# Kernel tuning notes

Hardware: AMD Instinct MI355X
Metric: run time of the kernel (lower is better)

The kernel has to match this reference:

```python
import jax, jax.numpy as jnp
import numpy as np

B, S, D = 2, 192, 256


def _clip_tangent(v, max_norm=4.0):
    n = jnp.linalg.norm(v, axis=-1, keepdims=True) + 1e-8
    return v * jnp.minimum(max_norm / n, 1.0)


def _sq(x):
    return jnp.sum(x * x, axis=-1, keepdims=True)


def _artanh(x):
    return jnp.arctanh(jnp.clip(x, -1.0 + 1e-7, 1.0 - 1e-7))


def _mobius_add(x, y):
    # Poincare ball (c=1) Mobius addition
    x2, y2 = _sq(x), _sq(y)
    xy = jnp.sum(x * y, axis=-1, keepdims=True)
    num = (1.0 + 2.0 * xy + y2) * x + (1.0 - x2) * y
    den = 1.0 + 2.0 * xy + x2 * y2
    return num / jnp.maximum(den, 1e-15)


def _expmap0(v):
    n = jnp.maximum(jnp.linalg.norm(v, axis=-1, keepdims=True), 1e-15)
    return jnp.tanh(n) * v / n


def _logmap0(x):
    n = jnp.maximum(jnp.linalg.norm(x, axis=-1, keepdims=True), 1e-15)
    return _artanh(n) * x / n


def _dist(x, y):
    u = _mobius_add(-x, y)
    return 2.0 * _artanh(jnp.linalg.norm(u, axis=-1))


def _logmap(x, y):
    u = _mobius_add(-x, y)
    un = jnp.maximum(jnp.linalg.norm(u, axis=-1, keepdims=True), 1e-15)
    lam = 2.0 / jnp.maximum(1.0 - _sq(x), 1e-15)
    return (2.0 / lam) * _artanh(un) * u / un


def _expmap(x, v):
    n = jnp.maximum(jnp.linalg.norm(v, axis=-1, keepdims=True), 1e-15)
    lam = 2.0 / jnp.maximum(1.0 - _sq(x), 1e-15)
    return _mobius_add(x, jnp.tanh(lam * n / 2.0) * v / n)


def _projx(x):
    n = jnp.linalg.norm(x, axis=-1, keepdims=True)
    maxn = 1.0 - 1e-5
    return jnp.where(n > maxn, x * maxn / jnp.maximum(n, 1e-15), x)


def _normalize(v, axis, eps=1e-8):
    return v / jnp.maximum(jnp.linalg.norm(v, axis=axis, keepdims=True), eps)


def setup_inputs() -> dict:
    key = jax.random.key(0)
    ks = jax.random.split(key, 8)

    def lin_w(k):
        return 0.02 * jax.random.normal(k, (D, D), jnp.float32)

    return {
        'q_in': 0.1 * jax.random.normal(ks[0], (B, S, D), jnp.float32),
        'k_in': 0.1 * jax.random.normal(ks[1], (B, S, D), jnp.float32),
        'v_in': 0.1 * jax.random.normal(ks[2], (B, S, D), jnp.float32),
        'Wq': lin_w(ks[3]), 'bq': jnp.zeros((D,), jnp.float32),
        'Wk': lin_w(ks[4]), 'bk': jnp.zeros((D,), jnp.float32),
        'Wv': lin_w(ks[5]), 'bv': jnp.zeros((D,), jnp.float32),
        'Wo': lin_w(ks[6]), 'bo': jnp.zeros((D,), jnp.float32),
        'tau': jnp.asarray(0.02, jnp.float32),
        'tangent_scale': jnp.asarray(1.0, jnp.float32),
    }


def _forward(q_in, k_in, v_in, Wq, bq, Wk, bk, Wv, bv, Wo, bo, tau, tangent_scale):
    nk = jax.random.split(jax.random.key(42), 3)  # deterministic stand-in for randn_like noise
    q = q_in @ Wq.T + bq
    k = k_in @ Wk.T + bk
    v = v_in @ Wv.T + bv

    q_hyp = _expmap0(_clip_tangent(q))
    k_hyp = _expmap0(_clip_tangent(k))

    # pairwise hyperbolic distance attention: [B,S,S]
    dist_matrix = _dist(q_hyp[:, :, None, :], k_hyp[:, None, :, :])
    min_dist = jnp.min(dist_matrix, axis=-1, keepdims=True)
    w_unnorm = jnp.exp(-(dist_matrix - min_dist))
    w_probs = w_unnorm / (jnp.sum(w_unnorm, axis=-1, keepdims=True) + 1e-8)
    h = jnp.einsum('bqs,bsd->bqd', w_probs, v)

    # differentiable Karcher flow (3-step Riemannian SGD for Frechet mean)
    wn = w_unnorm / (jnp.sum(w_unnorm, axis=-1, keepdims=True) + 1e-8)
    mu_hyp = _expmap0(_clip_tangent(jnp.einsum('bqs,bsd->bqd', wn, k)))
    k_hyp2 = _expmap0(_clip_tangent(k))
    for _ in range(3):
        log_k = _logmap(mu_hyp[:, :, None, :], k_hyp2[:, None, :, :])  # [B,S,S,D]
        v_grad = jnp.sum(wn[..., None] * log_k, axis=2)
        mu_hyp = _expmap(mu_hyp, _clip_tangent(0.1 * v_grad))

    noise = 1e-5 * jax.random.normal(nk[0], mu_hyp.shape, mu_hyp.dtype)
    k_centroid = _projx(mu_hyp + noise)

    c2k = _dist(k_centroid[:, :, None, :], k_hyp[:, None, :, :])  # [B,S,S]
    wv = w_unnorm / (jnp.sum(w_unnorm, axis=-1, keepdims=True) + 1e-8)
    entropy = -jnp.sum(wv * jnp.log(wv + 1e-8), axis=-1, keepdims=True)
    effective_mass = jnp.exp(entropy)
    variance = jnp.sum(wv * c2k ** 2, axis=-1, keepdims=True)
    tension = variance - tau * effective_mass  # [B,S,1]

    # local tangent frame + power iteration for principal direction
    k_local = _logmap(k_centroid[:, :, None, :], k_hyp[:, None, :, :])  # [B,S,S,D]
    weighted_k = k_local * jnp.sqrt(w_unnorm[..., None] + 1e-8)
    v_rand = jax.random.normal(nk[1], (B, S, D, 1), weighted_k.dtype)
    v_rand = _normalize(v_rand, axis=2)
    for _ in range(3):
        proj = jnp.einsum('bqsd,bqdo->bqso', weighted_k, v_rand)
        v_rand = _normalize(jnp.einsum('bqsd,bqso->bqdo', weighted_k, proj), axis=2)
    w_local = v_rand[..., 0]
    # transp0back(x, v) = v * lambda_x / 2 = v / (1 - ||x||^2)
    w_global = w_local / jnp.maximum(1.0 - _sq(k_centroid), 1e-15)
    fallback = _normalize(_logmap0(q_hyp) - _logmap0(k_centroid), axis=-1)
    w_proj = jnp.where(variance > 1e-5, w_global, fallback)

    h_norm = jnp.linalg.norm(h, axis=-1, keepdims=True)
    h_comp = jnp.arcsinh(h_norm) * h / (h_norm + 1e-8)

    # Pitchfork bifurcation ODE, RK4: dx/dt = tension*x - x^3
    x = jnp.sum(h_comp * w_proj, axis=-1, keepdims=True)
    ode_noise = 1e-4 * jax.random.normal(nk[2], x.shape, x.dtype)
    xi = jnp.where(x == 0, ode_noise, x)
    dt = 0.5
    f = lambda z: tension * z - z ** 3
    for _ in range(4):
        k1 = dt * f(xi)
        k2 = dt * f(xi + k1 / 2)
        k3 = dt * f(xi + k2 / 2)
        k4 = dt * f(xi + k3)
        xi = xi + (k1 + 2 * k2 + 2 * k3 + k4) / 6.0
    h_prime = h_comp + (xi - x) * w_proj
    h_prime_hyp = _expmap0(_clip_tangent(h_prime * tangent_scale))
    h_out_bif = _logmap0(h_prime_hyp)

    tau_safe = jnp.maximum(tau, 1e-3)
    gate = jnp.maximum(jnp.tanh(tension / tau_safe), 0.0)
    h_fused = (1.0 - gate) * h + gate * h_out_bif
    return h_fused @ Wo.T + bo


def reference(q_in, k_in, v_in, Wq, bq, Wk, bk, Wv, bv, Wo, bo, tau, tangent_scale):
    return _forward(q_in, k_in, v_in, Wq, bq, Wk, bk, Wv, bv, Wo, bo, tau, tangent_scale)
```

## Files before the change

kernel.cpp:

```cpp
#include <hip/hip_runtime.h>
#include <hip/hip_bf16.h>
#include <stdint.h>

#define BB 2
#define SS 192
#define DD 256
#define NROW (BB * SS)
#define NE (NROW * DD)

__device__ __forceinline__ uint32_t rotl32(uint32_t v, int d) {
  return (v << d) | (v >> (32 - d));
}

__device__ inline void threefry2x32(uint32_t k0, uint32_t k1, uint32_t x0, uint32_t x1,
                                    uint32_t* o0, uint32_t* o1) {
  uint32_t ks2 = k0 ^ k1 ^ 0x1BD11BDAu;
  x0 += k0; x1 += k1;
  const int ra[4] = {13, 15, 26, 6};
  const int rb[4] = {17, 29, 16, 24};
#pragma unroll
  for (int i = 0; i < 4; i++) { x0 += x1; x1 = rotl32(x1, ra[i]); x1 ^= x0; }
  x0 += k1; x1 += ks2 + 1u;
#pragma unroll
  for (int i = 0; i < 4; i++) { x0 += x1; x1 = rotl32(x1, rb[i]); x1 ^= x0; }
// ... 41 lines not shown

__device__ inline float jax_normal_from_bits(uint32_t bits) {
  float f = __uint_as_float((bits >> 9) | 0x3f800000u) - 1.0f;
  const float lo = -0.99999994f;
  float u = f * (1.0f - lo) + lo;
  u = fmaxf(lo, u);
  return 1.4142135623730951f * erfinv_xla_f32(u);
}

__device__ inline float jax_normal_at(uint32_t ka, uint32_t kb, uint32_t i) {
  uint32_t o0, o1;
  threefry2x32(ka, kb, 0u, i, &o0, &o1);
  return jax_normal_from_bits(o0 ^ o1);
}

__device__ inline double blockSum(double v, double* red, int tid) {
#pragma unroll
  for (int o = 32; o > 0; o >>= 1) v += __shfl_down(v, o, 64);
  __syncthreads();
  if ((tid & 63) == 0) red[tid >> 6] = v;
  __syncthreads();
  return (red[0] + red[1]) + (red[2] + red[3]);
}

__device__ inline double reduceS_sum(const double* arr, double* red, int tid) {
  __syncthreads();
  if (tid < 64) {
    double v = arr[tid] + arr[tid + 64] + arr[tid + 128];
#pragma unroll
    for (int o = 32; o > 0; o >>= 1) v += __shfl_down(v, o, 64);
    if (tid == 0) red[4] = v;
  }
  __syncthreads();
  return red[4];
}

__device__ inline double reduceS_min(const double* arr, double* red, int tid) {
  __syncthreads();
  if (tid < 64) {
    double v = fmin(arr[tid], fmin(arr[tid + 64], arr[tid + 128]));
#pragma unroll
    for (int o = 32; o > 0; o >>= 1) v = fmin(v, __shfl_down(v, o, 64));
    if (tid == 0) red[5] = v;
  }
  __syncthreads();
  return red[5];
}

#define SDOT(vecLds, khTp, outv) do {                                        \
    const float* cb_ = (khTp) + tid;                                         \
    double s0_=0.0,s1_=0.0,s2_=0.0,s3_=0.0,s4_=0.0,s5_=0.0,s6_=0.0,s7_=0.0;  \
    for (int d0_ = 0; d0_ < DD; d0_ += 8) {                                  \
      float f0_ = cb_[(size_t)(d0_ + 0) * SS];                               \
      float f1_ = cb_[(size_t)(d0_ + 1) * SS];                               \
      float f2_ = cb_[(size_t)(d0_ + 2) * SS];                               \
      float f3_ = cb_[(size_t)(d0_ + 3) * SS];                               \
      float f4_ = cb_[(size_t)(d0_ + 4) * SS];                               \
      float f5_ = cb_[(size_t)(d0_ + 5) * SS];                               \
      float f6_ = cb_[(size_t)(d0_ + 6) * SS];                               \
      float f7_ = cb_[(size_t)(d0_ + 7) * SS];                               \
      s0_ += (vecLds)[d0_ + 0] * (double)f0_;                                \
      s1_ += (vecLds)[d0_ + 1] * (double)f1_;                                \
      s2_ += (vecLds)[d0_ + 2] * (double)f2_;                                \
      s3_ += (vecLds)[d0_ + 3] * (double)f3_;                                \
      s4_ += (vecLds)[d0_ + 4] * (double)f4_;                                \
      s5_ += (vecLds)[d0_ + 5] * (double)f5_;                                \
      s6_ += (vecLds)[d0_ + 6] * (double)f6_;                                \
      s7_ += (vecLds)[d0_ + 7] * (double)f7_;                                \
    }                                                                        \
    (outv) = ((s0_ + s1_) + (s2_ + s3_)) + ((s4_ + s5_) + (s6_ + s7_));      \
  } while (0)

#define DSUM(wArr, mat, outv) do {                                           \
    const float* mb_ = (mat) + tid;                                          \
    double s0_=0.0,s1_=0.0,s2_=0.0,s3_=0.0,s4_=0.0,s5_=0.0,s6_=0.0,s7_=0.0;  \
    for (int t0_ = 0; t0_ < SS; t0_ += 8) {                                  \
      float f0_ = mb_[(size_t)(t0_ + 0) * DD];                               \
      float f1_ = mb_[(size_t)(t0_ + 1) * DD];                               \
      float f2_ = mb_[(size_t)(t0_ + 2) * DD];                               \
      float f3_ = mb_[(size_t)(t0_ + 3) * DD];                               \
      float f4_ = mb_[(size_t)(t0_ + 4) * DD];                               \
      float f5_ = mb_[(size_t)(t0_ + 5) * DD];                               \
      float f6_ = mb_[(size_t)(t0_ + 6) * DD];                               \
      float f7_ = mb_[(size_t)(t0_ + 7) * DD];                               \
      s0_ += (wArr)[t0_ + 0] * (double)f0_;                                  \
      s1_ += (wArr)[t0_ + 1] * (double)f1_;                                  \
      s2_ += (wArr)[t0_ + 2] * (double)f2_;                                  \
      s3_ += (wArr)[t0_ + 3] * (double)f3_;                                  \
      s4_ += (wArr)[t0_ + 4] * (double)f4_;                                  \
      s5_ += (wArr)[t0_ + 5] * (double)f5_;                                  \
      s6_ += (wArr)[t0_ + 6] * (double)f6_;                                  \
      s7_ += (wArr)[t0_ + 7] * (double)f7_;                                  \
    }                                                                        \
    (outv) = ((s0_ + s1_) + (s2_ + s3_)) + ((s4_ + s5_) + (s6_ + s7_));      \
  } while (0)

__global__ void transpose4(const float* __restrict__ Wq, const float* __restrict__ Wk,
                           const float* __restrict__ Wv, const float* __restrict__ Wo,
                           float* __restrict__ WqT, float* __restrict__ WkT,
                           float* __restrict__ WvT, float* __restrict__ WoT) {
  int m = blockIdx.x >> 8;
  int i = blockIdx.x & 255;
  int j = threadIdx.x;
  const float* S_; float* D_;
  if (m == 0) { S_ = Wq; D_ = WqT; }
  else if (m == 1) { S_ = Wk; D_ = WkT; }
  else if (m == 2) { S_ = Wv; D_ = WvT; }
  else { S_ = Wo; D_ = WoT; }
  D_[i * DD + j] = S_[j * DD + i];
}

__device__ inline double colDot(const float* __restrict__ xs,
                                const float* __restrict__ WT, int j) {
  const float* cb = WT + j;
  double s0=0.0,s1=0.0,s2=0.0,s3=0.0,s4=0.0,s5=0.0,s6=0.0,s7=0.0;
  for (int i0 = 0; i0 < DD; i0 += 8) {
    float f0 = cb[(size_t)(i0 + 0) * DD];
    float f1 = cb[(size_t)(i0 + 1) * DD];
    float f2 = cb[(size_t)(i0 + 2) * DD];
    float f3 = cb[(size_t)(i0 + 3) * DD];
    float f4 = cb[(size_t)(i0 + 4) * DD];
    float f5 = cb[(size_t)(i0 + 5) * DD];
    float f6 = cb[(size_t)(i0 + 6) * DD];
    float f7 = cb[(size_t)(i0 + 7) * DD];
    s0 += (double)xs[i0 + 0] * (double)f0;
    s1 += (double)xs[i0 + 1] * (double)f1;
    s2 += (double)xs[i0 + 2] * (double)f2;
    s3 += (double)xs[i0 + 3] * (double)f3;
    s4 += (double)xs[i0 + 4] * (double)f4;
    s5 += (double)xs[i0 + 5] * (double)f5;
    s6 += (double)xs[i0 + 6] * (double)f6;
    s7 += (double)xs[i0 + 7] * (double)f7;
  }
  return ((s0 + s1) + (s2 + s3)) + ((s4 + s5) + (s6 + s7));
}

__global__ __launch_bounds__(256) void proj_kernel(
    const float* __restrict__ q_in, const float* __restrict__ k_in, const float* __restrict__ v_in,
    const float* __restrict__ WqT, const float* __restrict__ WkT, const float* __restrict__ WvT,
    const float* __restrict__ bq, const float* __restrict__ bk, const float* __restrict__ bv,
    float* __restrict__ qh, float* __restrict__ kb, float* __restrict__ vb,
    float* __restrict__ kh, float* __restrict__ khT, double* __restrict__ y2g) {
  const int row = blockIdx.x, m = blockIdx.y, j = threadIdx.x;
  __shared__ float xs[DD];
  __shared__ double red[8];
  const float* x; const float* WT; const float* bias;
  if (m == 0) { x = q_in; WT = WqT; bias = bq; }
  else if (m == 1) { x = k_in; WT = WkT; bias = bk; }
  else { x = v_in; WT = WvT; bias = bv; }
  xs[j] = x[(size_t)row * DD + j];
  __syncthreads();
// ... 14 lines not shown
    kh[(size_t)row * DD + j] = khf;
    int bb = row / SS, s = row % SS;
    khT[((size_t)bb * DD + j) * SS + s] = khf;
    double y2 = blockSum((double)khf * (double)khf, red, j);
    if (j == 0) y2g[row] = y2;
  }
}

__global__ __launch_bounds__(256) void resonance_main(
    const float* __restrict__ q_hyp, const float* __restrict__ k_hyp,
    const float* __restrict__ k_hypT, const float* __restrict__ kmat,
    const float* __restrict__ vmat, const double* __restrict__ y2g,
    const float* __restrict__ WoT, const float* __restrict__ bo,
    const float* __restrict__ tau_p, const float* __restrict__ ts_p,
    float* __restrict__ out) {
  __shared__ double xq[DD], xc[DD], vr[DD];
  __shared__ double y2s[SS], wun[SS], wns[SS], alf[SS], bet[SS], sA[SS], sB[SS];
  __shared__ float hfl[DD];
  __shared__ double red[8];
  const int tid = threadIdx.x;
  const int blk = blockIdx.x;
  const int b = blk / SS;
  const size_t rowOff = (size_t)blk * DD;
  const float* khB = k_hyp + (size_t)b * SS * DD;
  const float* khT = k_hypT + (size_t)b * DD * SS;
  const float* kB = kmat + (size_t)b * SS * DD;
  const float* vB = vmat + (size_t)b * SS * DD;

  uint32_t nk0a, nk0b, nk1a, nk1b, nk2a, nk2b;
  threefry2x32(0u, 42u, 0u, 0u, &nk0a, &nk0b);
  threefry2x32(0u, 42u, 0u, 1u, &nk1a, &nk1b);
  threefry2x32(0u, 42u, 0u, 2u, &nk2a, &nk2b);
  const uint32_t ei = (uint32_t)(rowOff + tid);
  const double noiseval = 1e-5 * (double)jax_normal_at(nk0a, nk0b, ei);
  const double vrndval = (double)jax_normal_at(nk1a, nk1b, ei);
  const double odeval = 1e-4 * (double)jax_normal_at(nk2a, nk2b, (uint32_t)blk);

  double xqv = (double)q_hyp[rowOff + tid];
  xq[tid] = xqv;
  if (tid < SS) y2s[tid] = y2g[b * SS + tid];
  double x2q = blockSum(xqv * xqv, red, tid);

  if (tid < SS) {
    double dot;
    SDOT(xq, khT, dot);
    double y2 = y2s[tid];
    double A = 1.0 - 2.0 * dot + y2;
    double Dn = fmax(1.0 - 2.0 * dot + x2q * y2, 1e-15);
    double Bc = 1.0 - x2q;
    double u2 = (A * A * x2q - 2.0 * A * Bc * dot + Bc * Bc * y2) / (Dn * Dn);
    double unr = sqrt(fmax(u2, 0.0));
    sA[tid] = 2.0 * atanh(fmin(unr, 1.0 - 1e-7));
  }
  double mind = reduceS_min(sA, red, tid);
  if (tid < SS) wun[tid] = exp(-(sA[tid] - mind));
  double wsum = reduceS_sum(wun, red, tid);
  if (tid < SS) wns[tid] = wun[tid] * (1.0 / (wsum + 1e-8));
  __syncthreads();

  double hreg, mu;
  {
    const float* vb_ = vB + tid;
    const float* kb_ = kB + tid;
    double h0=0.0,h1=0.0,h2=0.0,h3=0.0, m0=0.0,m1=0.0,m2=0.0,m3=0.0;
    for (int s0 = 0; s0 < SS; s0 += 4) {
      float v0 = vb_[(size_t)(s0 + 0) * DD];
      float v1 = vb_[(size_t)(s0 + 1) * DD];
      float v2 = vb_[(size_t)(s0 + 2) * DD];
      float v3 = vb_[(size_t)(s0 + 3) * DD];
      float k0 = kb_[(size_t)(s0 + 0) * DD];
      float k1 = kb_[(size_t)(s0 + 1) * DD];
      float k2 = kb_[(size_t)(s0 + 2) * DD];
      float k3 = kb_[(size_t)(s0 + 3) * DD];
      double w0 = wns[s0 + 0], w1 = wns[s0 + 1], w2 = wns[s0 + 2], w3 = wns[s0 + 3];
      h0 += w0 * (double)v0; h1 += w1 * (double)v1;
      h2 += w2 * (double)v2; h3 += w3 * (double)v3;
      m0 += w0 * (double)k0; m1 += w1 * (double)k1;
      m2 += w2 * (double)k2; m3 += w3 * (double)k3;
    }
    hreg = (h0 + h1) + (h2 + h3);
    mu = (m0 + m1) + (m2 + m3);
  }

  double x2c;
  {
    double n2 = blockSum(mu * mu, red, tid);
    double n = sqrt(n2);
    double cf = fmin(4.0 / (n + 1e-8), 1.0);
    double ncl = fmax(n * cf, 1e-15);
    double th = tanh(ncl);
    xc[tid] = mu * (th * cf / ncl);
    x2c = th * th;
  }
  __syncthreads();

  for (int it = 0; it < 3; ++it) {
    if (tid < SS) {
      double dot;
      SDOT(xc, khT, dot);
      double y2 = y2s[tid];
      double A = 1.0 - 2.0 * dot + y2;
      double Dn = fmax(1.0 - 2.0 * dot + x2c * y2, 1e-15);
      double Bc = 1.0 - x2c;
      double u2 = (A * A * x2c - 2.0 * A * Bc * dot + Bc * Bc * y2) / (Dn * Dn);
      double unr = sqrt(fmax(u2, 0.0));
      double un = fmax(unr, 1e-15);
      double coef = fmax(Bc, 1e-15) * atanh(fmin(un, 1.0 - 1e-7)) / un;
      double cs = wns[tid] * coef / Dn;
      sA[tid] = cs;
      sB[tid] = cs * A;
    }
    double S1 = reduceS_sum(sB, red, tid);
    double g;
    DSUM(sA, khB, g);
    double xold = xc[tid];
    double Bc = 1.0 - x2c;
    double vg = Bc * g - S1 * xold;
    double nv2 = blockSum(vg * vg, red, tid);
    double nv = 0.1 * sqrt(nv2);
    double cf = fmin(4.0 / (nv + 1e-8), 1.0);
    double nw = fmax(nv * cf, 1e-15);
    double tsc = tanh(nw / fmax(Bc, 1e-15));
    double zco = tsc * 0.1 * cf / nw;
    double z = zco * vg;
    double xz = blockSum(xold * z, red, tid);
    double z2 = tsc * tsc;
    double den = fmax(1.0 + 2.0 * xz + x2c * z2, 1e-15);
    double xnew = ((1.0 + 2.0 * xz + z2) * xold + (1.0 - x2c) * z) / den;
    xc[tid] = xnew;
    x2c = blockSum(xnew * xnew, red, tid);
  }

  {
    double cn = xc[tid] + noiseval;
    double n2 = blockSum(cn * cn, red, tid);
    double nn = sqrt(n2);
    if (nn > 1.0 - 1e-5) cn *= (1.0 - 1e-5) / fmax(nn, 1e-15);
    xc[tid] = cn;
    x2c = blockSum(cn * cn, red, tid);
  }

  if (tid < SS) {
    double dot;
    SDOT(xc, khT, dot);
    double y2 = y2s[tid];
    double A = 1.0 - 2.0 * dot + y2;
    double Dn = fmax(1.0 - 2.0 * dot + x2c * y2, 1e-15);
    double Bc = 1.0 - x2c;
    double u2 = (A * A * x2c - 2.0 * A * Bc * dot + Bc * Bc * y2) / (Dn * Dn);
    double unr = sqrt(fmax(u2, 0.0));
    double c2k = 2.0 * atanh(fmin(unr, 1.0 - 1e-7));
    sA[tid] = wns[tid] * c2k * c2k;
    sB[tid] = -wns[tid] * log(wns[tid] + 1e-8);
    double un = fmax(unr, 1e-15);
    double gl = fmax(Bc, 1e-15) * atanh(fmin(un, 1.0 - 1e-7)) / (un * Dn);
    double sq = sqrt(wun[tid] + 1e-8);
    alf[tid] = -sq * gl * A;
    bet[tid] = sq * gl * Bc;
  }
  double variance = reduceS_sum(sA, red, tid);
  double entropy = reduceS_sum(sB, red, tid);
  double tau = (double)tau_p[0];
  double tension = variance - tau * exp(entropy);

  {
    double n2 = blockSum(vrndval * vrndval, red, tid);
    vr[tid] = vrndval / fmax(sqrt(n2), 1e-8);
  }
  for (int it = 0; it < 3; ++it) {
    double dxv = blockSum(xc[tid] * vr[tid], red, tid);
    if (tid < SS) {
      double dot;
      SDOT(vr, khT, dot);
      double pj = alf[tid] * dxv + bet[tid] * dot;
      sA[tid] = alf[tid] * pj;
      sB[tid] = bet[tid] * pj;
    }
    double T1 = reduceS_sum(sA, red, tid);
    double g;
    DSUM(sB, khB, g);
    double vnew = T1 * xc[tid] + g;
    double n2 = blockSum(vnew * vnew, red, tid);
    vr[tid] = vnew / fmax(sqrt(n2), 1e-8);
  }

  double wproj;
  {
    double wg = vr[tid] / fmax(1.0 - x2c, 1e-15);
    double nq = fmax(sqrt(x2q), 1e-15);
    double aq = atanh(fmin(nq, 1.0 - 1e-7)) / nq;
    double nc = fmax(sqrt(x2c), 1e-15);
    double ac = atanh(fmin(nc, 1.0 - 1e-7)) / nc;
    double f = aq * xq[tid] - ac * xc[tid];
    double n2 = blockSum(f * f, red, tid);
    double fb = f / fmax(sqrt(n2), 1e-8);
    wproj = (variance > 1e-5) ? wg : fb;
  }

  double hn2 = blockSum(hreg * hreg, red, tid);
  double hn = sqrt(hn2);
  double hsc = asinh(hn) / (hn + 1e-8);
  double hc = hsc * hreg;
  double x = blockSum(hc * wproj, red, tid);
  double xi = (x == 0.0) ? odeval : x;
  const double dt = 0.5;
#pragma unroll
  for (int r = 0; r < 4; ++r) {
    double k1 = dt * (tension * xi - xi * xi * xi);
    double a2 = xi + 0.5 * k1;
    double k2 = dt * (tension * a2 - a2 * a2 * a2);
    double a3 = xi + 0.5 * k2;
    double k3 = dt * (tension * a3 - a3 * a3 * a3);
    double a4 = xi + k3;
    double k4 = dt * (tension * a4 - a4 * a4 * a4);
    xi += (k1 + 2.0 * k2 + 2.0 * k3 + k4) / 6.0;
  }
  double ts = (double)ts_p[0];
  double hp = (hc + (xi - x) * wproj) * ts;
  double hp2 = blockSum(hp * hp, red, tid);
  double nhp = sqrt(hp2);
  double cf = fmin(4.0 / (nhp + 1e-8), 1.0);
  double ncl = fmax(nhp * cf, 1e-15);
  double th = tanh(ncl);
  double nb = fmax(th, 1e-15);
  double ab = atanh(fmin(nb, 1.0 - 1e-7)) / nb;
  double hob = ab * th * cf / ncl * hp;
  double gate = fmax(tanh(tension / fmax(tau, 1e-3)), 0.0);

  hfl[tid] = (float)((1.0 - gate) * hreg + gate * hob);
  __syncthreads();
  double o = colDot(hfl, WoT, tid) + (double)bo[tid];
  out[rowOff + tid] = (float)o;
}

extern "C" void kernel_launch(void* const* d_in, const int* in_sizes, int n_in,
                              void* d_out, int out_size, void* d_ws, size_t ws_size,
                              hipStream_t stream) {
  const float* q_in = (const float*)d_in[0];
  const float* k_in = (const float*)d_in[1];
  const float* v_in = (const float*)d_in[2];
  const float* Wq = (const float*)d_in[3];
  const float* bq = (const float*)d_in[4];
  const float* Wk = (const float*)d_in[5];
  const float* bk = (const float*)d_in[6];
  const float* Wv = (const float*)d_in[7];
  const float* bv = (const float*)d_in[8];
  const float* Wo = (const float*)d_in[9];
// ... 14 lines not shown
  float* WkT = (float*)alloc((size_t)DD * DD * 4);
  float* WvT = (float*)alloc((size_t)DD * DD * 4);
  float* WoT = (float*)alloc((size_t)DD * DD * 4);
  float* kb = (float*)alloc((size_t)NE * 4);
  float* vb = (float*)alloc((size_t)NE * 4);
  float* qh = (float*)alloc((size_t)NE * 4);
  float* kh = (float*)alloc((size_t)NE * 4);
  float* khT = (float*)alloc((size_t)NE * 4);
  double* y2g = (double*)alloc((size_t)NROW * 8);

  hipLaunchKernelGGL(transpose4, dim3(4 * DD), dim3(DD), 0, stream,
                     Wq, Wk, Wv, Wo, WqT, WkT, WvT, WoT);
  hipLaunchKernelGGL(proj_kernel, dim3(NROW, 3), dim3(DD), 0, stream,
                     q_in, k_in, v_in, WqT, WkT, WvT, bq, bk, bv,
                     qh, kb, vb, kh, khT, y2g);
  hipLaunchKernelGGL(resonance_main, dim3(NROW), dim3(DD), 0, stream,
                     qh, kh, khT, kb, vb, y2g, WoT, bo, tau, ts, out);
}
```

Before: 144.3 us.

## Process two query rows per block in resonance kernel to share key loads

The main kernel now handles two adjacent query rows per block, so every load of the key, value and weight matrices feeds two sets of accumulators. Reductions are paired, which halves the number of barriers per row. The aim is to cut global/L2 traffic on the memory-bound dot products and amortise synchronisation. The cost is half as many blocks (192 instead of 384), higher register and LDS pressure, and lower occupancy on a GPU with many CUs.

```diff
diff --git a/kernel.cpp b/kernel.cpp
--- a/kernel.cpp
+++ b/kernel.cpp
@@ -79,42 +79,58 @@
   return jax_normal_from_bits(o0 ^ o1);
 }
 
-__device__ inline double blockSum(double v, double* red, int tid) {
-#pragma unroll
-  for (int o = 32; o > 0; o >>= 1) v += __shfl_down(v, o, 64);
-  __syncthreads();
-  if ((tid & 63) == 0) red[tid >> 6] = v;
-  __syncthreads();
-  return (red[0] + red[1]) + (red[2] + red[3]);
-}
-
-__device__ inline double reduceS_sum(const double* arr, double* red, int tid) {
+__device__ inline void blockSum2(double vA, double vB, double* red, int tid,
+                                 double& oA, double& oB) {
+#pragma unroll
+  for (int o = 32; o > 0; o >>= 1) {
+    vA += __shfl_down(vA, o, 64);
+    vB += __shfl_down(vB, o, 64);
+  }
+  __syncthreads();
+  if ((tid & 63) == 0) { red[tid >> 6] = vA; red[4 + (tid >> 6)] = vB; }
+  __syncthreads();
+  oA = (red[0] + red[1]) + (red[2] + red[3]);
+  oB = (red[4] + red[5]) + (red[6] + red[7]);
+}
+
+__device__ inline void reduceS_sum2(const double* aA, const double* aB, double* red,
+                                    int tid, double& oA, double& oB) {
   __syncthreads();
   if (tid < 64) {
-    double v = arr[tid] + arr[tid + 64] + arr[tid + 128];
-#pragma unroll
-    for (int o = 32; o > 0; o >>= 1) v += __shfl_down(v, o, 64);
-    if (tid == 0) red[4] = v;
-  }
-  __syncthreads();
-  return red[4];
-}
-
-__device__ inline double reduceS_min(const double* arr, double* red, int tid) {
+    double vA = aA[tid] + aA[tid + 64] + aA[tid + 128];
+    double vB = aB[tid] + aB[tid + 64] + aB[tid + 128];
+#pragma unroll
+    for (int o = 32; o > 0; o >>= 1) {
+      vA += __shfl_down(vA, o, 64);
+      vB += __shfl_down(vB, o, 64);
+    }
+    if (tid == 0) { red[8] = vA; red[9] = vB; }
+  }
+  __syncthreads();
+  oA = red[8]; oB = red[9];
+}
+
+__device__ inline void reduceS_min2(const double* aA, const double* aB, double* red,
+                                    int tid, double& oA, double& oB) {
   __syncthreads();
   if (tid < 64) {
-    double v = fmin(arr[tid], fmin(arr[tid + 64], arr[tid + 128]));
-#pragma unroll
-    for (int o = 32; o > 0; o >>= 1) v = fmin(v, __shfl_down(v, o, 64));
-    if (tid == 0) red[5] = v;
-  }
-  __syncthreads();
-  return red[5];
-}
-
-#define SDOT(vecLds, khTp, outv) do {                                        \
+    double vA = fmin(aA[tid], fmin(aA[tid + 64], aA[tid + 128]));
+    double vB = fmin(aB[tid], fmin(aB[tid + 64], aB[tid + 128]));
+#pragma unroll
+    for (int o = 32; o > 0; o >>= 1) {
+      vA = fmin(vA, __shfl_down(vA, o, 64));
+      vB = fmin(vB, __shfl_down(vB, o, 64));
+    }
+    if (tid == 0) { red[10] = vA; red[11] = vB; }
+  }
+  __syncthreads();
+  oA = red[10]; oB = red[11];
+}
+
+#define SDOT2(vLA, vLB, khTp, outA, outB) do {                               \
     const float* cb_ = (khTp) + tid;                                         \
-    double s0_=0.0,s1_=0.0,s2_=0.0,s3_=0.0,s4_=0.0,s5_=0.0,s6_=0.0,s7_=0.0;  \
+    double a0_=0,a1_=0,a2_=0,a3_=0,a4_=0,a5_=0,a6_=0,a7_=0;                  \
+    double b0_=0,b1_=0,b2_=0,b3_=0,b4_=0,b5_=0,b6_=0,b7_=0;                  \
     for (int d0_ = 0; d0_ < DD; d0_ += 8) {                                  \
       float f0_ = cb_[(size_t)(d0_ + 0) * SS];                               \
       float f1_ = cb_[(size_t)(d0_ + 1) * SS];                               \
@@ -124,21 +140,23 @@
       float f5_ = cb_[(size_t)(d0_ + 5) * SS];                               \
       float f6_ = cb_[(size_t)(d0_ + 6) * SS];                               \
       float f7_ = cb_[(size_t)(d0_ + 7) * SS];                               \
-      s0_ += (vecLds)[d0_ + 0] * (double)f0_;                                \
-      s1_ += (vecLds)[d0_ + 1] * (double)f1_;                                \
-      s2_ += (vecLds)[d0_ + 2] * (double)f2_;                                \
-      s3_ += (vecLds)[d0_ + 3] * (double)f3_;                                \
-      s4_ += (vecLds)[d0_ + 4] * (double)f4_;                                \
-      s5_ += (vecLds)[d0_ + 5] * (double)f5_;                                \
-      s6_ += (vecLds)[d0_ + 6] * (double)f6_;                                \
-      s7_ += (vecLds)[d0_ + 7] * (double)f7_;                                \
+      a0_ += (vLA)[d0_ + 0] * (double)f0_;  b0_ += (vLB)[d0_ + 0] * (double)f0_; \
+      a1_ += (vLA)[d0_ + 1] * (double)f1_;  b1_ += (vLB)[d0_ + 1] * (double)f1_; \
+      a2_ += (vLA)[d0_ + 2] * (double)f2_;  b2_ += (vLB)[d0_ + 2] * (double)f2_; \
+      a3_ += (vLA)[d0_ + 3] * (double)f3_;  b3_ += (vLB)[d0_ + 3] * (double)f3_; \
+      a4_ += (vLA)[d0_ + 4] * (double)f4_;  b4_ += (vLB)[d0_ + 4] * (double)f4_; \
+      a5_ += (vLA)[d0_ + 5] * (double)f5_;  b5_ += (vLB)[d0_ + 5] * (double)f5_; \
+      a6_ += (vLA)[d0_ + 6] * (double)f6_;  b6_ += (vLB)[d0_ + 6] * (double)f6_; \
+      a7_ += (vLA)[d0_ + 7] * (double)f7_;  b7_ += (vLB)[d0_ + 7] * (double)f7_; \
     }                                                                        \
-    (outv) = ((s0_ + s1_) + (s2_ + s3_)) + ((s4_ + s5_) + (s6_ + s7_));      \
+    (outA) = ((a0_ + a1_) + (a2_ + a3_)) + ((a4_ + a5_) + (a6_ + a7_));      \
+    (outB) = ((b0_ + b1_) + (b2_ + b3_)) + ((b4_ + b5_) + (b6_ + b7_));      \
   } while (0)
 
-#define DSUM(wArr, mat, outv) do {                                           \
-    const float* mb_ = (mat) + tid;                                          \
-    double s0_=0.0,s1_=0.0,s2_=0.0,s3_=0.0,s4_=0.0,s5_=0.0,s6_=0.0,s7_=0.0;  \
+#define DSUM2(wA, wB, mat, outA, outB) do {                                  \
+    const float* mb_ = (mat);                                                \
+    double a0_=0,a1_=0,a2_=0,a3_=0,a4_=0,a5_=0,a6_=0,a7_=0;                  \
+    double b0_=0,b1_=0,b2_=0,b3_=0,b4_=0,b5_=0,b6_=0,b7_=0;                  \
     for (int t0_ = 0; t0_ < SS; t0_ += 8) {                                  \
       float f0_ = mb_[(size_t)(t0_ + 0) * DD];                               \
       float f1_ = mb_[(size_t)(t0_ + 1) * DD];                               \
@@ -148,16 +166,17 @@
       float f5_ = mb_[(size_t)(t0_ + 5) * DD];                               \
       float f6_ = mb_[(size_t)(t0_ + 6) * DD];                               \
       float f7_ = mb_[(size_t)(t0_ + 7) * DD];                               \
-      s0_ += (wArr)[t0_ + 0] * (double)f0_;                                  \
-      s1_ += (wArr)[t0_ + 1] * (double)f1_;                                  \
-      s2_ += (wArr)[t0_ + 2] * (double)f2_;                                  \
-      s3_ += (wArr)[t0_ + 3] * (double)f3_;                                  \
-      s4_ += (wArr)[t0_ + 4] * (double)f4_;                                  \
-      s5_ += (wArr)[t0_ + 5] * (double)f5_;                                  \
-      s6_ += (wArr)[t0_ + 6] * (double)f6_;                                  \
-      s7_ += (wArr)[t0_ + 7] * (double)f7_;                                  \
+      a0_ += (wA)[t0_ + 0] * (double)f0_;  b0_ += (wB)[t0_ + 0] * (double)f0_; \
+      a1_ += (wA)[t0_ + 1] * (double)f1_;  b1_ += (wB)[t0_ + 1] * (double)f1_; \
+      a2_ += (wA)[t0_ + 2] * (double)f2_;  b2_ += (wB)[t0_ + 2] * (double)f2_; \
+      a3_ += (wA)[t0_ + 3] * (double)f3_;  b3_ += (wB)[t0_ + 3] * (double)f3_; \
+      a4_ += (wA)[t0_ + 4] * (double)f4_;  b4_ += (wB)[t0_ + 4] * (double)f4_; \
+      a5_ += (wA)[t0_ + 5] * (double)f5_;  b5_ += (wB)[t0_ + 5] * (double)f5_; \
+      a6_ += (wA)[t0_ + 6] * (double)f6_;  b6_ += (wB)[t0_ + 6] * (double)f6_; \
+      a7_ += (wA)[t0_ + 7] * (double)f7_;  b7_ += (wB)[t0_ + 7] * (double)f7_; \
     }                                                                        \
-    (outv) = ((s0_ + s1_) + (s2_ + s3_)) + ((s4_ + s5_) + (s6_ + s7_));      \
+    (outA) = ((a0_ + a1_) + (a2_ + a3_)) + ((a4_ + a5_) + (a6_ + a7_));      \
+    (outB) = ((b0_ + b1_) + (b2_ + b3_)) + ((b4_ + b5_) + (b6_ + b7_));      \
   } while (0)
 
 __global__ void transpose4(const float* __restrict__ Wq, const float* __restrict__ Wk,
@@ -173,6 +192,15 @@
   else if (m == 2) { S_ = Wv; D_ = WvT; }
   else { S_ = Wo; D_ = WoT; }
   D_[i * DD + j] = S_[j * DD + i];
+}
+
+__device__ inline double blockSum(double v, double* red, int tid) {
+#pragma unroll
+  for (int o = 32; o > 0; o >>= 1) v += __shfl_down(v, o, 64);
+  __syncthreads();
+  if ((tid & 63) == 0) red[tid >> 6] = v;
+  __syncthreads();
+  return (red[0] + red[1]) + (red[2] + red[3]);
 }
 
 __device__ inline double colDot(const float* __restrict__ xs,
@@ -200,6 +228,25 @@
   return ((s0 + s1) + (s2 + s3)) + ((s4 + s5) + (s6 + s7));
 }
 
+__device__ inline void colDot2(const float* __restrict__ xsA, const float* __restrict__ xsB,
+                               const float* __restrict__ WT, int j,
+                               double& oA, double& oB) {
+  const float* cb = WT + j;
+  double a0=0,a1=0,a2=0,a3=0, b0=0,b1=0,b2=0,b3=0;
+  for (int i0 = 0; i0 < DD; i0 += 4) {
+    float f0 = cb[(size_t)(i0 + 0) * DD];
+    float f1 = cb[(size_t)(i0 + 1) * DD];
+    float f2 = cb[(size_t)(i0 + 2) * DD];
+    float f3 = cb[(size_t)(i0 + 3) * DD];
+    a0 += (double)xsA[i0 + 0] * (double)f0;  b0 += (double)xsB[i0 + 0] * (double)f0;
+    a1 += (double)xsA[i0 + 1] * (double)f1;  b1 += (double)xsB[i0 + 1] * (double)f1;
+    a2 += (double)xsA[i0 + 2] * (double)f2;  b2 += (double)xsB[i0 + 2] * (double)f2;
+    a3 += (double)xsA[i0 + 3] * (double)f3;  b3 += (double)xsB[i0 + 3] * (double)f3;
+  }
+  oA = (a0 + a1) + (a2 + a3);
+  oB = (b0 + b1) + (b2 + b3);
+}
+
 __global__ __launch_bounds__(256) void proj_kernel(
     const float* __restrict__ q_in, const float* __restrict__ k_in, const float* __restrict__ v_in,
     const float* __restrict__ WqT, const float* __restrict__ WkT, const float* __restrict__ WvT,
@@ -244,14 +291,19 @@
     const float* __restrict__ WoT, const float* __restrict__ bo,
     const float* __restrict__ tau_p, const float* __restrict__ ts_p,
     float* __restrict__ out) {
-  __shared__ double xq[DD], xc[DD], vr[DD];
-  __shared__ double y2s[SS], wun[SS], wns[SS], alf[SS], bet[SS], sA[SS], sB[SS];
-  __shared__ float hfl[DD];
-  __shared__ double red[8];
+  __shared__ double xqA[DD], xqB[DD], xcA[DD], xcB[DD], vrA[DD], vrB[DD];
+  __shared__ double y2s[SS];
+  __shared__ double wunA[SS], wunB[SS], wnsA[SS], wnsB[SS];
+  __shared__ double alfA[SS], alfB[SS], betA[SS], betB[SS];
+  __shared__ double sAA[SS], sAB[SS], sBA[SS], sBB[SS];
+  __shared__ float hflA[DD], hflB[DD];
+  __shared__ double red[16];
   const int tid = threadIdx.x;
-  const int blk = blockIdx.x;
-  const int b = blk / SS;
-  const size_t rowOff = (size_t)blk * DD;
+  const int pblk = blockIdx.x;
+  const int b = pblk / (SS / 2);
+  const int qp = pblk % (SS / 2);
+  const int rowA = b * SS + 2 * qp, rowB = rowA + 1;
+  const size_t offA = (size_t)rowA * DD, offB = (size_t)rowB * DD;
   const float* khB = k_hyp + (size_t)b * SS * DD;
   const float* khT = k_hypT + (size_t)b * DD * SS;
   const float* kB = kmat + (size_t)b * SS * DD;
@@ -261,38 +313,61 @@
   threefry2x32(0u, 42u, 0u, 0u, &nk0a, &nk0b);
   threefry2x32(0u, 42u, 0u, 1u, &nk1a, &nk1b);
   threefry2x32(0u, 42u, 0u, 2u, &nk2a, &nk2b);
-  const uint32_t ei = (uint32_t)(rowOff + tid);
-  const double noiseval = 1e-5 * (double)jax_normal_at(nk0a, nk0b, ei);
-  const double vrndval = (double)jax_normal_at(nk1a, nk1b, ei);
-  const double odeval = 1e-4 * (double)jax_normal_at(nk2a, nk2b, (uint32_t)blk);
-
-  double xqv = (double)q_hyp[rowOff + tid];
-  xq[tid] = xqv;
+  const double noiseA = 1e-5 * (double)jax_normal_at(nk0a, nk0b, (uint32_t)(offA + tid));
+  const double noiseB = 1e-5 * (double)jax_normal_at(nk0a, nk0b, (uint32_t)(offB + tid));
+  const double vrndA = (double)jax_normal_at(nk1a, nk1b, (uint32_t)(offA + tid));
+  const double vrndB = (double)jax_normal_at(nk1a, nk1b, (uint32_t)(offB + tid));
+  const double odeA = 1e-4 * (double)jax_normal_at(nk2a, nk2b, (uint32_t)rowA);
+  const double odeB = 1e-4 * (double)jax_normal_at(nk2a, nk2b, (uint32_t)rowB);
+
+  double xqvA = (double)q_hyp[offA + tid];
+  double xqvB = (double)q_hyp[offB + tid];
+  xqA[tid] = xqvA;
+  xqB[tid] = xqvB;
   if (tid < SS) y2s[tid] = y2g[b * SS + tid];
-  double x2q = blockSum(xqv * xqv, red, tid);
+  double x2qA, x2qB;
+  blockSum2(xqvA * xqvA, xqvB * xqvB, red, tid, x2qA, x2qB);
 
   if (tid < SS) {
-    double dot;
-    SDOT(xq, khT, dot);
+    double dA, dB;
+    SDOT2(xqA, xqB, khT, dA, dB);
     double y2 = y2s[tid];
-    double A = 1.0 - 2.0 * dot + y2;
-    double Dn = fmax(1.0 - 2.0 * dot + x2q * y2, 1e-15);
-    double Bc = 1.0 - x2q;
-    double u2 = (A * A * x2q - 2.0 * A * Bc * dot + Bc * Bc * y2) / (Dn * Dn);
-    double unr = sqrt(fmax(u2, 0.0));
-    sA[tid] = 2.0 * atanh(fmin(unr, 1.0 - 1e-7));
-  }
-  double mind = reduceS_min(sA, red, tid);
-  if (tid < SS) wun[tid] = exp(-(sA[tid] - mind));
-  double wsum = reduceS_sum(wun, red, tid);
-  if (tid < SS) wns[tid] = wun[tid] * (1.0 / (wsum + 1e-8));
-  __syncthreads();
-
-  double hreg, mu;
+    {
+      double A = 1.0 - 2.0 * dA + y2;
+      double Dn = fmax(1.0 - 2.0 * dA + x2qA * y2, 1e-15);
+      double Bc = 1.0 - x2qA;
+      double u2 = (A * A * x2qA - 2.0 * A * Bc * dA + Bc * Bc * y2) / (Dn * Dn);
+      double unr = sqrt(fmax(u2, 0.0));
+      sAA[tid] = 2.0 * atanh(fmin(unr, 1.0 - 1e-7));
+    }
+    {
+      double A = 1.0 - 2.0 * dB + y2;
+      double Dn = fmax(1.0 - 2.0 * dB + x2qB * y2, 1e-15);
+      double Bc = 1.0 - x2qB;
+      double u2 = (A * A * x2qB - 2.0 * A * Bc * dB + Bc * Bc * y2) / (Dn * Dn);
+      double unr = sqrt(fmax(u2, 0.0));
+      sAB[tid] = 2.0 * atanh(fmin(unr, 1.0 - 1e-7));
+    }
+  }
+  double mindA, mindB;
+  reduceS_min2(sAA, sAB, red, tid, mindA, mindB);
+  if (tid < SS) {
+    wunA[tid] = exp(-(sAA[tid] - mindA));
+    wunB[tid] = exp(-(sAB[tid] - mindB));
+  }
+  double wsA, wsB;
+  reduceS_sum2(wunA, wunB, red, tid, wsA, wsB);
+  if (tid < SS) {
+    wnsA[tid] = wunA[tid] * (1.0 / (wsA + 1e-8));
+    wnsB[tid] = wunB[tid] * (1.0 / (wsB + 1e-8));
+  }
+  __syncthreads();
+
+  double hregA, hregB, muA, muB;
   {
     const float* vb_ = vB + tid;
     const float* kb_ = kB + tid;
-    double h0=0.0,h1=0.0,h2=0.0,h3=0.0, m0=0.0,m1=0.0,m2=0.0,m3=0.0;
+    double hA0=0,hA1=0,hB0=0,hB1=0, mA0=0,mA1=0,mB0=0,mB1=0;
     for (int s0 = 0; s0 < SS; s0 += 4) {
       float v0 = vb_[(size_t)(s0 + 0) * DD];
       float v1 = vb_[(size_t)(s0 + 1) * DD];
@@ -302,165 +377,291 @@
       float k1 = kb_[(size_t)(s0 + 1) * DD];
       float k2 = kb_[(size_t)(s0 + 2) * DD];
       float k3 = kb_[(size_t)(s0 + 3) * DD];
-      double w0 = wns[s0 + 0], w1 = wns[s0 + 1], w2 = wns[s0 + 2], w3 = wns[s0 + 3];
-      h0 += w0 * (double)v0; h1 += w1 * (double)v1;
-      h2 += w2 * (double)v2; h3 += w3 * (double)v3;
-      m0 += w0 * (double)k0; m1 += w1 * (double)k1;
-      m2 += w2 * (double)k2; m3 += w3 * (double)k3;
-    }
-    hreg = (h0 + h1) + (h2 + h3);
-    mu = (m0 + m1) + (m2 + m3);
-  }
-
-  double x2c;
+      double wA0 = wnsA[s0 + 0], wA1 = wnsA[s0 + 1], wA2 = wnsA[s0 + 2], wA3 = wnsA[s0 + 3];
+      double wB0 = wnsB[s0 + 0], wB1 = wnsB[s0 + 1], wB2 = wnsB[s0 + 2], wB3 = wnsB[s0 + 3];
+      hA0 += wA0 * (double)v0; hB0 += wB0 * (double)v0;
+      mA0 += wA0 * (double)k0; mB0 += wB0 * (double)k0;
+      hA1 += wA1 * (double)v1; hB1 += wB1 * (double)v1;
+      mA1 += wA1 * (double)k1; mB1 += wB1 * (double)k1;
+      hA0 += wA2 * (double)v2; hB0 += wB2 * (double)v2;
+      mA0 += wA2 * (double)k2; mB0 += wB2 * (double)k2;
+      hA1 += wA3 * (double)v3; hB1 += wB3 * (double)v3;
+      mA1 += wA3 * (double)k3; mB1 += wB3 * (double)k3;
+    }
+    hregA = hA0 + hA1; hregB = hB0 + hB1;
+    muA = mA0 + mA1;   muB = mB0 + mB1;
+  }
+
+  double x2cA, x2cB;
   {
-    double n2 = blockSum(mu * mu, red, tid);
-    double n = sqrt(n2);
-    double cf = fmin(4.0 / (n + 1e-8), 1.0);
-    double ncl = fmax(n * cf, 1e-15);
-    double th = tanh(ncl);
-    xc[tid] = mu * (th * cf / ncl);
-    x2c = th * th;
+    double n2A, n2B;
+    blockSum2(muA * muA, muB * muB, red, tid, n2A, n2B);
+    {
+      double n = sqrt(n2A);
+      double cf = fmin(4.0 / (n + 1e-8), 1.0);
+      double ncl = fmax(n * cf, 1e-15);
+      double th = tanh(ncl);
+      xcA[tid] = muA * (th * cf / ncl);
+      x2cA = th * th;
+    }
+    {
+      double n = sqrt(n2B);
+      double cf = fmin(4.0 / (n + 1e-8), 1.0);
+      double ncl = fmax(n * cf, 1e-15);
+      double th = tanh(ncl);
+      xcB[tid] = muB * (th * cf / ncl);
+      x2cB = th * th;
+    }
   }
   __syncthreads();
 
   for (int it = 0; it < 3; ++it) {
     if (tid < SS) {
-      double dot;
-      SDOT(xc, khT, dot);
+      double dA, dB;
+      SDOT2(xcA, xcB, khT, dA, dB);
       double y2 = y2s[tid];
-      double A = 1.0 - 2.0 * dot + y2;
-      double Dn = fmax(1.0 - 2.0 * dot + x2c * y2, 1e-15);
-      double Bc = 1.0 - x2c;
-      double u2 = (A * A * x2c - 2.0 * A * Bc * dot + Bc * Bc * y2) / (Dn * Dn);
+      {
+        double A = 1.0 - 2.0 * dA + y2;
+        double Dn = fmax(1.0 - 2.0 * dA + x2cA * y2, 1e-15);
+        double Bc = 1.0 - x2cA;
+        double u2 = (A * A * x2cA - 2.0 * A * Bc * dA + Bc * Bc * y2) / (Dn * Dn);
+        double unr = sqrt(fmax(u2, 0.0));
+        double un = fmax(unr, 1e-15);
+        double coef = fmax(Bc, 1e-15) * atanh(fmin(un, 1.0 - 1e-7)) / un;
+        double cs = wnsA[tid] * coef / Dn;
+        sAA[tid] = cs;
+        sBA[tid] = cs * A;
+      }
+      {
+        double A = 1.0 - 2.0 * dB + y2;
+        double Dn = fmax(1.0 - 2.0 * dB + x2cB * y2, 1e-15);
+        double Bc = 1.0 - x2cB;
+        double u2 = (A * A * x2cB - 2.0 * A * Bc * dB + Bc * Bc * y2) / (Dn * Dn);
+        double unr = sqrt(fmax(u2, 0.0));
+        double un = fmax(unr, 1e-15);
+        double coef = fmax(Bc, 1e-15) * atanh(fmin(un, 1.0 - 1e-7)) / un;
+        double cs = wnsB[tid] * coef / Dn;
+        sAB[tid] = cs;
+        sBB[tid] = cs * A;
+      }
+    }
+    double S1A, S1B;
+    reduceS_sum2(sBA, sBB, red, tid, S1A, S1B);
+    double gA, gB;
+    DSUM2(sAA, sAB, khB + tid, gA, gB);
+    double xoldA = xcA[tid], xoldB = xcB[tid];
+    double BcA = 1.0 - x2cA, BcB = 1.0 - x2cB;
+    double vgA = BcA * gA - S1A * xoldA;
+    double vgB = BcB * gB - S1B * xoldB;
+    double nv2A, nv2B;
+    blockSum2(vgA * vgA, vgB * vgB, red, tid, nv2A, nv2B);
+    double zA, z2A, zB, z2B;
+    {
+      double nv = 0.1 * sqrt(nv2A);
+      double cf = fmin(4.0 / (nv + 1e-8), 1.0);
+      double nw = fmax(nv * cf, 1e-15);
+      double tsc = tanh(nw / fmax(BcA, 1e-15));
+      zA = tsc * 0.1 * cf / nw * vgA;
+      z2A = tsc * tsc;
+    }
+    {
+      double nv = 0.1 * sqrt(nv2B);
+      double cf = fmin(4.0 / (nv + 1e-8), 1.0);
+      double nw = fmax(nv * cf, 1e-15);
+      double tsc = tanh(nw / fmax(BcB, 1e-15));
+      zB = tsc * 0.1 * cf / nw * vgB;
+      z2B = tsc * tsc;
+    }
+    double xzA, xzB;
+    blockSum2(xoldA * zA, xoldB * zB, red, tid, xzA, xzB);
+    double xnewA = ((1.0 + 2.0 * xzA + z2A) * xoldA + (1.0 - x2cA) * zA) /
+                   fmax(1.0 + 2.0 * xzA + x2cA * z2A, 1e-15);
+    double xnewB = ((1.0 + 2.0 * xzB + z2B) * xoldB + (1.0 - x2cB) * zB) /
+                   fmax(1.0 + 2.0 * xzB + x2cB * z2B, 1e-15);
+    xcA[tid] = xnewA;
+    xcB[tid] = xnewB;
+    blockSum2(xnewA * xnewA, xnewB * xnewB, red, tid, x2cA, x2cB);
+  }
+
+  {
+    double cnA = xcA[tid] + noiseA;
+    double cnB = xcB[tid] + noiseB;
+    double n2A, n2B;
+    blockSum2(cnA * cnA, cnB * cnB, red, tid, n2A, n2B);
+    double nnA = sqrt(n2A), nnB = sqrt(n2B);
+    if (nnA > 1.0 - 1e-5) cnA *= (1.0 - 1e-5) / fmax(nnA, 1e-15);
+    if (nnB > 1.0 - 1e-5) cnB *= (1.0 - 1e-5) / fmax(nnB, 1e-15);
+    xcA[tid] = cnA;
+    xcB[tid] = cnB;
+    blockSum2(cnA * cnA, cnB * cnB, red, tid, x2cA, x2cB);
+  }
+
+  if (tid < SS) {
+    double dA, dB;
+    SDOT2(xcA, xcB, khT, dA, dB);
+    double y2 = y2s[tid];
+    {
+      double A = 1.0 - 2.0 * dA + y2;
+      double Dn = fmax(1.0 - 2.0 * dA + x2cA * y2, 1e-15);
+      double Bc = 1.0 - x2cA;
+      double u2 = (A * A * x2cA - 2.0 * A * Bc * dA + Bc * Bc * y2) / (Dn * Dn);
       double unr = sqrt(fmax(u2, 0.0));
+      double c2k = 2.0 * atanh(fmin(unr, 1.0 - 1e-7));
+      sAA[tid] = wnsA[tid] * c2k * c2k;
+      sBA[tid] = -wnsA[tid] * log(wnsA[tid] + 1e-8);
       double un = fmax(unr, 1e-15);
-      double coef = fmax(Bc, 1e-15) * atanh(fmin(un, 1.0 - 1e-7)) / un;
-      double cs = wns[tid] * coef / Dn;
-      sA[tid] = cs;
-      sB[tid] = cs * A;
-    }
-    double S1 = reduceS_sum(sB, red, tid);
-    double g;
-    DSUM(sA, khB, g);
-    double xold = xc[tid];
-    double Bc = 1.0 - x2c;
-    double vg = Bc * g - S1 * xold;
-    double nv2 = blockSum(vg * vg, red, tid);
-    double nv = 0.1 * sqrt(nv2);
-    double cf = fmin(4.0 / (nv + 1e-8), 1.0);
-    double nw = fmax(nv * cf, 1e-15);
-    double tsc = tanh(nw / fmax(Bc, 1e-15));
-    double zco = tsc * 0.1 * cf / nw;
-    double z = zco * vg;
-    double xz = blockSum(xold * z, red, tid);
-    double z2 = tsc * tsc;
-    double den = fmax(1.0 + 2.0 * xz + x2c * z2, 1e-15);
-    double xnew = ((1.0 + 2.0 * xz + z2) * xold + (1.0 - x2c) * z) / den;
-    xc[tid] = xnew;
-    x2c = blockSum(xnew * xnew, red, tid);
-  }
+      double gl = fmax(Bc, 1e-15) * atanh(fmin(un, 1.0 - 1e-7)) / (un * Dn);
+      double sq = sqrt(wunA[tid] + 1e-8);
+      alfA[tid] = -sq * gl * A;
+      betA[tid] = sq * gl * Bc;
+    }
+    {
+      double A = 1.0 - 2.0 * dB + y2;
+      double Dn = fmax(1.0 - 2.0 * dB + x2cB * y2, 1e-15);
+      double Bc = 1.0 - x2cB;
+      double u2 = (A * A * x2cB - 2.0 * A * Bc * dB + Bc * Bc * y2) / (Dn * Dn);
+      double unr = sqrt(fmax(u2, 0.0));
+      double c2k = 2.0 * atanh(fmin(unr, 1.0 - 1e-7));
+      sAB[tid] = wnsB[tid] * c2k * c2k;
+      sBB[tid] = -wnsB[tid] * log(wnsB[tid] + 1e-8);
+      double un = fmax(unr, 1e-15);
+      double gl = fmax(Bc, 1e-15) * atanh(fmin(un, 1.0 - 1e-7)) / (un * Dn);
+      double sq = sqrt(wunB[tid] + 1e-8);
+      alfB[tid] = -sq * gl * A;
+      betB[tid] = sq * gl * Bc;
+    }
+  }
+  double varA, varB, entA, entB;
+  reduceS_sum2(sAA, sAB, red, tid, varA, varB);
+  reduceS_sum2(sBA, sBB, red, tid, entA, entB);
+  double tau = (double)tau_p[0];
+  double tensionA = varA - tau * exp(entA);
+  double tensionB = varB - tau * exp(entB);
 
   {
-    double cn = xc[tid] + noiseval;
-    double n2 = blockSum(cn * cn, red, tid);
-    double nn = sqrt(n2);
-    if (nn > 1.0 - 1e-5) cn *= (1.0 - 1e-5) / fmax(nn, 1e-15);
-    xc[tid] = cn;
-    x2c = blockSum(cn * cn, red, tid);
-  }
-
-  if (tid < SS) {
-    double dot;
-    SDOT(xc, khT, dot);
-    double y2 = y2s[tid];
-    double A = 1.0 - 2.0 * dot + y2;
-    double Dn = fmax(1.0 - 2.0 * dot + x2c * y2, 1e-15);
-    double Bc = 1.0 - x2c;
-    double u2 = (A * A * x2c - 2.0 * A * Bc * dot + Bc * Bc * y2) / (Dn * Dn);
-    double unr = sqrt(fmax(u2, 0.0));
-    double c2k = 2.0 * atanh(fmin(unr, 1.0 - 1e-7));
-    sA[tid] = wns[tid] * c2k * c2k;
-    sB[tid] = -wns[tid] * log(wns[tid] + 1e-8);
-    double un = fmax(unr, 1e-15);
-    double gl = fmax(Bc, 1e-15) * atanh(fmin(un, 1.0 - 1e-7)) / (un * Dn);
-    double sq = sqrt(wun[tid] + 1e-8);
-    alf[tid] = -sq * gl * A;
-    bet[tid] = sq * gl * Bc;
-  }
-  double variance = reduceS_sum(sA, red, tid);
-  double entropy = reduceS_sum(sB, red, tid);
-  double tau = (double)tau_p[0];
-  double tension = variance - tau * exp(entropy);
-
+    double n2A, n2B;
+    blockSum2(vrndA * vrndA, vrndB * vrndB, red, tid, n2A, n2B);
+    vrA[tid] = vrndA / fmax(sqrt(n2A), 1e-8);
+    vrB[tid] = vrndB / fmax(sqrt(n2B), 1e-8);
+  }
+  for (int it = 0; it < 3; ++it) {
+    double dxvA, dxvB;
+    blockSum2(xcA[tid] * vrA[tid], xcB[tid] * vrB[tid], red, tid, dxvA, dxvB);
+    if (tid < SS) {
+      double dA, dB;
+      SDOT2(vrA, vrB, khT, dA, dB);
+      double pjA = alfA[tid] * dxvA + betA[tid] * dA;
+      double pjB = alfB[tid] * dxvB + betB[tid] * dB;
+      sAA[tid] = alfA[tid] * pjA;
+      sBA[tid] = betA[tid] * pjA;
+      sAB[tid] = alfB[tid] * pjB;
+      sBB[tid] = betB[tid] * pjB;
+    }
+    double T1A, T1B;
+    reduceS_sum2(sAA, sAB, red, tid, T1A, T1B);
+    double gA, gB;
+    DSUM2(sBA, sBB, khB + tid, gA, gB);
+    double vnewA = T1A * xcA[tid] + gA;
+    double vnewB = T1B * xcB[tid] + gB;
+    double n2A, n2B;
+    blockSum2(vnewA * vnewA, vnewB * vnewB, red, tid, n2A, n2B);
+    vrA[tid] = vnewA / fmax(sqrt(n2A), 1e-8);
+    vrB[tid] = vnewB / fmax(sqrt(n2B), 1e-8);
+  }
+
+  double wprojA, wprojB;
   {
-    double n2 = blockSum(vrndval * vrndval, red, tid);
-    vr[tid] = vrndval / fmax(sqrt(n2), 1e-8);
-  }
-  for (int it = 0; it < 3; ++it) {
-    double dxv = blockSum(xc[tid] * vr[tid], red, tid);
-    if (tid < SS) {
-      double dot;
-      SDOT(vr, khT, dot);
-      double pj = alf[tid] * dxv + bet[tid] * dot;
-      sA[tid] = alf[tid] * pj;
-      sB[tid] = bet[tid] * pj;
-    }
-    double T1 = reduceS_sum(sA, red, tid);
-    double g;
-    DSUM(sB, khB, g);
-    double vnew = T1 * xc[tid] + g;
-    double n2 = blockSum(vnew * vnew, red, tid);
-    vr[tid] = vnew / fmax(sqrt(n2), 1e-8);
-  }
-
-  double wproj;
+    double fA, fB;
+    {
+      double nq = fmax(sqrt(x2qA), 1e-15);
+      double aq = atanh(fmin(nq, 1.0 - 1e-7)) / nq;
+      double nc = fmax(sqrt(x2cA), 1e-15);
+      double ac = atanh(fmin(nc, 1.0 - 1e-7)) / nc;
+      fA = aq * xqA[tid] - ac * xcA[tid];
+    }
+    {
+      double nq = fmax(sqrt(x2qB), 1e-15);
+      double aq = atanh(fmin(nq, 1.0 - 1e-7)) / nq;
+      double nc = fmax(sqrt(x2cB), 1e-15);
+      double ac = atanh(fmin(nc, 1.0 - 1e-7)) / nc;
+      fB = aq * xqB[tid] - ac * xcB[tid];
+    }
+    double n2A, n2B;
+    blockSum2(fA * fA, fB * fB, red, tid, n2A, n2B);
+    double wgA = vrA[tid] / fmax(1.0 - x2cA, 1e-15);
+    double wgB = vrB[tid] / fmax(1.0 - x2cB, 1e-15);
+    wprojA = (varA > 1e-5) ? wgA : (fA / fmax(sqrt(n2A), 1e-8));
+    wprojB = (varB > 1e-5) ? wgB : (fB / fmax(sqrt(n2B), 1e-8));
+  }
+
+  double hn2A, hn2B;
+  blockSum2(hregA * hregA, hregB * hregB, red, tid, hn2A, hn2B);
+  double hnA = sqrt(hn2A), hnB = sqrt(hn2B);
+  double hcA = asinh(hnA) / (hnA + 1e-8) * hregA;
+  double hcB = asinh(hnB) / (hnB + 1e-8) * hregB;
+  double xA, xB;
+  blockSum2(hcA * wprojA, hcB * wprojB, red, tid, xA, xB);
+  double xiA = (xA == 0.0) ? odeA : xA;
+  double xiB = (xB == 0.0) ? odeB : xB;
+  const double dt = 0.5;
+#pragma unroll
+  for (int r = 0; r < 4; ++r) {
+    {
+      double k1 = dt * (tensionA * xiA - xiA * xiA * xiA);
+      double a2 = xiA + 0.5 * k1;
+      double k2 = dt * (tensionA * a2 - a2 * a2 * a2);
+      double a3 = xiA + 0.5 * k2;
+      double k3 = dt * (tensionA * a3 - a3 * a3 * a3);
+      double a4 = xiA + k3;
+      double k4 = dt * (tensionA * a4 - a4 * a4 * a4);
+      xiA += (k1 + 2.0 * k2 + 2.0 * k3 + k4) / 6.0;
+    }
+    {
+      double k1 = dt * (tensionB * xiB - xiB * xiB * xiB);
+      double a2 = xiB + 0.5 * k1;
+      double k2 = dt * (tensionB * a2 - a2 * a2 * a2);
+      double a3 = xiB + 0.5 * k2;
+      double k3 = dt * (tensionB * a3 - a3 * a3 * a3);
+      double a4 = xiB + k3;
+      double k4 = dt * (tensionB * a4 - a4 * a4 * a4);
+      xiB += (k1 + 2.0 * k2 + 2.0 * k3 + k4) / 6.0;
+    }
+  }
+  double ts = (double)ts_p[0];
+  double hpA = (hcA + (xiA - xA) * wprojA) * ts;
+  double hpB = (hcB + (xiB - xB) * wprojB) * ts;
+  double hp2A, hp2B;
+  blockSum2(hpA * hpA, hpB * hpB, red, tid, hp2A, hp2B);
+  double hobA, hobB;
   {
-    double wg = vr[tid] / fmax(1.0 - x2c, 1e-15);
-    double nq = fmax(sqrt(x2q), 1e-15);
-    double aq = atanh(fmin(nq, 1.0 - 1e-7)) / nq;
-    double nc = fmax(sqrt(x2c), 1e-15);
-    double ac = atanh(fmin(nc, 1.0 - 1e-7)) / nc;
-    double f = aq * xq[tid] - ac * xc[tid];
-    double n2 = blockSum(f * f, red, tid);
-    double fb = f / fmax(sqrt(n2), 1e-8);
-    wproj = (variance > 1e-5) ? wg : fb;
-  }
-
-  double hn2 = blockSum(hreg * hreg, red, tid);
-  double hn = sqrt(hn2);
-  double hsc = asinh(hn) / (hn + 1e-8);
-  double hc = hsc * hreg;
-  double x = blockSum(hc * wproj, red, tid);
-  double xi = (x == 0.0) ? odeval : x;
-  const double dt = 0.5;
-#pragma unroll
-  for (int r = 0; r < 4; ++r) {
-    double k1 = dt * (tension * xi - xi * xi * xi);
-    double a2 = xi + 0.5 * k1;
-    double k2 = dt * (tension * a2 - a2 * a2 * a2);
-    double a3 = xi + 0.5 * k2;
-    double k3 = dt * (tension * a3 - a3 * a3 * a3);
-    double a4 = xi + k3;
-    double k4 = dt * (tension * a4 - a4 * a4 * a4);
-    xi += (k1 + 2.0 * k2 + 2.0 * k3 + k4) / 6.0;
-  }
-  double ts = (double)ts_p[0];
-  double hp = (hc + (xi - x) * wproj) * ts;
-  double hp2 = blockSum(hp * hp, red, tid);
-  double nhp = sqrt(hp2);
-  double cf = fmin(4.0 / (nhp + 1e-8), 1.0);
-  double ncl = fmax(nhp * cf, 1e-15);
-  double th = tanh(ncl);
-  double nb = fmax(th, 1e-15);
-  double ab = atanh(fmin(nb, 1.0 - 1e-7)) / nb;
-  double hob = ab * th * cf / ncl * hp;
-  double gate = fmax(tanh(tension / fmax(tau, 1e-3)), 0.0);
-
-  hfl[tid] = (float)((1.0 - gate) * hreg + gate * hob);
-  __syncthreads();
-  double o = colDot(hfl, WoT, tid) + (double)bo[tid];
-  out[rowOff + tid] = (float)o;
+    double nhp = sqrt(hp2A);
+    double cf = fmin(4.0 / (nhp + 1e-8), 1.0);
+    double ncl = fmax(nhp * cf, 1e-15);
+    double th = tanh(ncl);
+    double nb = fmax(th, 1e-15);
+    double ab = atanh(fmin(nb, 1.0 - 1e-7)) / nb;
+    hobA = ab * th * cf / ncl * hpA;
+  }
+  {
+    double nhp = sqrt(hp2B);
+    double cf = fmin(4.0 / (nhp + 1e-8), 1.0);
+    double ncl = fmax(nhp * cf, 1e-15);
+    double th = tanh(ncl);
+    double nb = fmax(th, 1e-15);
+    double ab = atanh(fmin(nb, 1.0 - 1e-7)) / nb;
+    hobB = ab * th * cf / ncl * hpB;
+  }
+  double gateA = fmax(tanh(tensionA / fmax(tau, 1e-3)), 0.0);
+  double gateB = fmax(tanh(tensionB / fmax(tau, 1e-3)), 0.0);
+
+  hflA[tid] = (float)((1.0 - gateA) * hregA + gateA * hobA);
+  hflB[tid] = (float)((1.0 - gateB) * hregB + gateB * hobB);
+  __syncthreads();
+  double oA, oB;
+  colDot2(hflA, hflB, WoT, tid, oA, oB);
+  double bias = (double)bo[tid];
+  out[offA + tid] = (float)(oA + bias);
+  out[offB + tid] = (float)(oB + bias);
 }
 
 extern "C" void kernel_launch(void* const* d_in, const int* in_sizes, int n_in,
@@ -505,6 +706,6 @@
   hipLaunchKernelGGL(proj_kernel, dim3(NROW, 3), dim3(DD), 0, stream,
                      q_in, k_in, v_in, WqT, WkT, WvT, bq, bk, bv,
                      qh, kb, vb, kh, khT, y2g);
-  hipLaunchKernelGGL(resonance_main, dim3(NROW), dim3(DD), 0, stream,
+  hipLaunchKernelGGL(resonance_main, dim3(NROW / 2), dim3(DD), 0, stream,
                      qh, kh, khT, kb, vb, y2g, WoT, bo, tau, ts, out);
 }
```

After: 166.9 us. 15.7% more time.
